# Optimization experiments

Hardware: AMD Instinct MI355X
Metric: run time of the kernel (lower is better)

## Reference

```python
import jax, jax.numpy as jnp
import numpy as np

B, D_IN, U, E = 8192, 1024, 1024, 16

def setup_inputs() -> dict:
    key = jax.random.key(0)
    k1, k2, k3, k4 = jax.random.split(key, 4)
    inputs = jax.random.normal(k1, (B, D_IN), dtype=jnp.float32)
    # type_prob: probability over entity types per example, [B, E, 1]
    tp = jax.random.uniform(k2, (B, E, 1), dtype=jnp.float32)
    type_prob = tp / jnp.sum(tp, axis=1, keepdims=True)
    # Stacked per-entity Dense params: W [E, D_IN, U], b [E, U]
    scale = 1.0 / np.sqrt(D_IN)
    W = jax.random.normal(k3, (E, D_IN, U), dtype=jnp.float32) * scale
    b = jax.random.normal(k4, (E, U), dtype=jnp.float32) * 0.01
    return {"inputs": inputs, "type_prob": type_prob, "W": W, "b": b}

def reference(inputs, type_prob, W, b):
    # Per-entity Dense, batched as one einsum: [B, E, U]
    logits = jnp.einsum('bd,edu->beu', inputs, W) + b
    probs = jax.nn.softmax(logits, axis=-1)  # softmax over wp_units, per entity
    # transpose to [B, U, E], matmul with type_prob [B, E, 1], reduce_sum last axis
    # == weighted combine over entities: [B, U]
    result = jnp.einsum('beu,be->bu', probs, type_prob[..., 0])
    return result
```

## Files before the change

kernel.cpp:

```cpp
#include <hip/hip_runtime.h>
#include <hip/hip_bf16.h>
#include <hip/hip_fp16.h>
#include <stdint.h>

typedef _Float16 f16;
typedef _Float16 f16x4 __attribute__((ext_vector_type(4)));
typedef _Float16 f16x8 __attribute__((ext_vector_type(8)));
typedef float f32x4 __attribute__((ext_vector_type(4)));

#define NB 8192
#define ND 1024
#define NU 1024
#define NE 16

__global__ __launch_bounds__(256) void k_transpose_cast(const float* __restrict__ W,
                                                        f16* __restrict__ WT) {
  __shared__ f16 tile[64][68];
  const int e = blockIdx.z;
  const int u0 = blockIdx.x * 64;
  const int d0 = blockIdx.y * 64;
  const int t = threadIdx.x;
  const int r = t >> 4;
  const int c = (t & 15) << 2;
  const float* src = W + (size_t)e * ND * NU;
  f16* dst = WT + (size_t)e * NU * ND;
#pragma unroll
  for (int i = 0; i < 4; ++i) {
    const int rr = r + i * 16;
    const float4 v = *(const float4*)(src + (size_t)(d0 + rr) * NU + (u0 + c));
    tile[rr][c + 0] = (f16)v.x;
    tile[rr][c + 1] = (f16)v.y;
    tile[rr][c + 2] = (f16)v.z;
    tile[rr][c + 3] = (f16)v.w;
  }
  __syncthreads();
#pragma unroll
  for (int i = 0; i < 4; ++i) {
    const int rr = r + i * 16;
    f16x4 h;
    h[0] = tile[c + 0][rr];
    h[1] = tile[c + 1][rr];
    h[2] = tile[c + 2][rr];
    h[3] = tile[c + 3][rr];
    *(f16x4*)(dst + (size_t)(u0 + rr) * ND + (d0 + c)) = h;
  }
}

__global__ __launch_bounds__(256) void k_cast_x(const float* __restrict__ X,
                                                f16* __restrict__ Xh) {
  const size_t i = ((size_t)blockIdx.x * 256 + threadIdx.x) * 8;
  const float4 v0 = *(const float4*)(X + i);
  const float4 v1 = *(const float4*)(X + i + 4);
  f16x8 h;
  h[0] = (f16)v0.x; h[1] = (f16)v0.y; h[2] = (f16)v0.z; h[3] = (f16)v0.w;
  h[4] = (f16)v1.x; h[5] = (f16)v1.y; h[6] = (f16)v1.z; h[7] = (f16)v1.w;
  *(f16x8*)(Xh + i) = h;
}


typedef __attribute__((address_space(3))) void lds_void_t;
typedef __attribute__((address_space(1))) const void gbl_void_t;

__device__ __forceinline__ void gload16(const void* g, void* l) {
  __builtin_amdgcn_global_load_lds((gbl_void_t*)g, (lds_void_t*)l, 16, 0, 0);
}

#define GSTAGE(buf, kk)                                                        \
  {                                                                            \
    _Pragma("unroll") for (int i_ = 0; i_ < 4; ++i_) {                         \
      const unsigned s_ = i_ * 512 + t;                                        \
      const unsigned row_ = s_ >> 3, ch_ = s_ & 7;                             \
      const unsigned sch_ = ch_ ^ (row_ & 7);                                  \
      const unsigned lb_ = (i_ * 512 + (t & ~63u)) * 16;                       \
      gload16(Ag + (size_t)row_ * 2048 + (size_t)(kk) * 128 + sch_ * 16,       \
              smem + (buf) * 32768 + lb_);                                     \
      gload16(Bg + (size_t)row_ * 2048 + (size_t)(kk) * 128 + sch_ * 16,       \
              smem + 65536 + (buf) * 32768 + lb_);                             \
    }                                                                          \
  }

#define GCOMPUTE(buf)                                                          \
  _Pragma("unroll") for (int ks_ = 0; ks_ < 2; ++ks_) {                        \
    f16x8 bfr_[4];                                                             \
    _Pragma("unroll") for (int nb_ = 0; nb_ < 4; ++nb_) {                      \
      const unsigned U_ = wc * 64 + nb_ * 16 + ln;                             \
      const unsigned ch_ = (unsigned)(ks_ * 4 + g) ^ (U_ & 7);                 \
      bfr_[nb_] =                                                              \
          *(const f16x8*)(smem + 65536 + (buf) * 32768 + U_ * 128 + ch_ * 16); \
    }                                                                          \
    _Pragma("unroll") for (int mb_ = 0; mb_ < 8; ++mb_) {                      \
      const unsigned R_ = wr * 128 + mb_ * 16 + ln;                            \
      const unsigned ch_ = (unsigned)(ks_ * 4 + g) ^ (R_ & 7);                 \
      const f16x8 af_ =                                                        \
          *(const f16x8*)(smem + (buf) * 32768 + R_ * 128 + ch_ * 16);         \
      _Pragma("unroll") for (int nb_ = 0; nb_ < 4; ++nb_) {                    \
        acc[mb_][nb_] = __builtin_amdgcn_mfma_f32_16x16x32_f16(                \
            af_, bfr_[nb_], acc[mb_][nb_], 0, 0, 0);                           \
      }                                                                        \
    }                                                                          \
  }

__global__ __launch_bounds__(512, 2) void k_gemm_exp(const f16* __restrict__ Xc,
                                                     const f16* __restrict__ WT,
                                                     const float* __restrict__ BIAS,
                                                     f16* __restrict__ P,
                                                     float* __restrict__ S4,
                                                     int MTs, int CR) {
  __shared__ alignas(16) unsigned char smem[131072];

  const int t = threadIdx.x;
  const int w = t >> 6;
  const int l = t & 63;
  const int g = l >> 4;
  const int ln = l & 15;
  const int wr = w >> 2;
  const int wc = w & 3;

  const int bid = blockIdx.x;
  const int xcd = bid & 7;
  const int j = bid >> 3;
  const int ntl = j >> MTs;
  const int mt = j & ((1 << MTs) - 1);
  const int nt = xcd * 8 + ntl;

  const char* Ag = (const char*)Xc + (size_t)mt * 256 * 2048;
  const char* Bg = (const char*)WT + (size_t)nt * 256 * 2048;

  f32x4 acc[8][4];
#pragma unroll
  for (int mb = 0; mb < 8; ++mb)
#pragma unroll
    for (int nb = 0; nb < 4; ++nb) acc[mb][nb] = (f32x4){0.f, 0.f, 0.f, 0.f};

  GSTAGE(0, 0);
  __syncthreads();
#pragma unroll 1
  for (int kk = 0; kk < 16; ++kk) {
    const int buf = kk & 1;
    if (kk < 15) GSTAGE(buf ^ 1, kk + 1);
    __builtin_amdgcn_s_setprio(1);
    GCOMPUTE(buf);
    __builtin_amdgcn_s_setprio(0);
    __syncthreads();
  }

  float bv[4];
  const float* bp = BIAS + ((size_t)(nt >> 2) << 10) + (nt & 3) * 256 + wc * 64 + ln;
#pragma unroll
  for (int nb = 0; nb < 4; ++nb) bv[nb] = bp[nb * 16];

  float* red = (float*)smem;
  f16* Prow = P + (size_t)(mt * 256 + wr * 128) * 16384 + (size_t)nt * 256 + wc * 64 + ln;

#pragma unroll
  for (int mb = 0; mb < 8; ++mb) {
    float rs[4] = {0.f, 0.f, 0.f, 0.f};
#pragma unroll
    for (int nb = 0; nb < 4; ++nb) {
#pragma unroll
      for (int r = 0; r < 4; ++r) {
        const float p = __expf(acc[mb][nb][r] + bv[nb]);
        rs[r] += p;
        Prow[(size_t)(mb * 16 + g * 4 + r) * 16384 + nb * 16] = (f16)p;
      }
    }
#pragma unroll
    for (int r = 0; r < 4; ++r) {
      float v = rs[r];
      v += __shfl_xor(v, 1);
      v += __shfl_xor(v, 2);
      v += __shfl_xor(v, 4);
      v += __shfl_xor(v, 8);
      if (ln == 0) red[(wr * 128 + mb * 16 + g * 4 + r) * 4 + wc] = v;
    }
  }
  __syncthreads();
  if (t < 256) {
    const float s = (red[t * 4 + 0] + red[t * 4 + 1]) + (red[t * 4 + 2] + red[t * 4 + 3]);
    S4[(size_t)nt * CR + mt * 256 + t] = s;
  }
}

__global__ __launch_bounds__(512) void k_combine(const f16* __restrict__ P,
                                                 const float* __restrict__ TP,
                                                 const float* __restrict__ S4,
                                                 float* __restrict__ OUT,
                                                 int RB, int CR) {
  __shared__ float c_s[4][16];
  const int t = threadIdx.x;
  const int blk = blockIdx.x;
  if (t < 64) {
    const int rr = t >> 4, e = t & 15;
    const int bl = blk * 4 + rr;
    float S = 0.f;
#pragma unroll
    for (int q = 0; q < 4; ++q) S += S4[(size_t)(e * 4 + q) * CR + bl];
    c_s[rr][e] = TP[(size_t)(RB + bl) * NE + e] / S;
  }
  __syncthreads();
  const int rl = t >> 7;
  const int bl = blk * 4 + rl;
  const int u0 = (t & 127) * 8;
  float a[8] = {0.f, 0.f, 0.f, 0.f, 0.f, 0.f, 0.f, 0.f};
  const f16* Pb = P + (size_t)bl * 16384 + u0;
#pragma unroll
  for (int e = 0; e < NE; ++e) {
    const float c = c_s[rl][e];
    const f16x8 pv = *(const f16x8*)(Pb + e * 1024);
#pragma unroll
    for (int jj = 0; jj < 8; ++jj) a[jj] += c * (float)pv[jj];
  }
  float* op = OUT + (size_t)(RB + bl) * NU + u0;
  *(float4*)(op) = (float4){a[0], a[1], a[2], a[3]};
  *(float4*)(op + 4) = (float4){a[4], a[5], a[6], a[7]};
}

#define BM 64
#define BUH 512
#define NRT 128
#define WT_BYTES ((size_t)NE * NU * ND * 2)
#define SUMS_FLOATS ((size_t)NE * NRT * 2 * 64)
#define FLG_INTS ((size_t)NE * NRT * 2)

#define LOADB(F, soff)                                   \
  {                                                      \
    const char* p_ = wtc + (soff) + vbase;               \
    F[0] = *(const f16x8*)(p_);                          \
    F[1] = *(const f16x8*)(p_ + 1 * 16 * ND * 2);        \
    F[2] = *(const f16x8*)(p_ + 2 * 16 * ND * 2);        \
    F[3] = *(const f16x8*)(p_ + 3 * 16 * ND * 2);        \
  }

#define MFMA_HALF(F, kbyte)                                                         \
  {                                                                                 \
    const f16x8 a0 = *(const f16x8*)(A_s + (ln + 0) * 2064 + g * 16 + (kbyte));     \
    const f16x8 a1 = *(const f16x8*)(A_s + (ln + 16) * 2064 + g * 16 + (kbyte));    \
    const f16x8 a2 = *(const f16x8*)(A_s + (ln + 32) * 2064 + g * 16 + (kbyte));    \
    const f16x8 a3 = *(const f16x8*)(A_s + (ln + 48) * 2064 + g * 16 + (kbyte));    \
    _Pragma("unroll") for (int n_ = 0; n_ < 4; ++n_) {                              \
      acc[0][n_] = __builtin_amdgcn_mfma_f32_16x16x32_f16(a0, F[n_], acc[0][n_], 0, 0, 0); \
      acc[1][n_] = __builtin_amdgcn_mfma_f32_16x16x32_f16(a1, F[n_], acc[1][n_], 0, 0, 0); \
      acc[2][n_] = __builtin_amdgcn_mfma_f32_16x16x32_f16(a2, F[n_], acc[2][n_], 0, 0, 0); \
      acc[3][n_] = __builtin_amdgcn_mfma_f32_16x16x32_f16(a3, F[n_], acc[3][n_], 0, 0, 0); \
    }                                                                               \
  }

__device__ __forceinline__ size_t wt_soff(int L) {
  L = (L > 511) ? 511 : L;
  return (size_t)(L >> 5) * ((size_t)NU * ND * 2) + (size_t)(L & 31) * 64;
}

__global__ __launch_bounds__(512, 2) void k_proj(const float* __restrict__ X,
                                                 const float* __restrict__ TP,
                                                 const f16* __restrict__ WT,
                                                 const float* __restrict__ BIAS,
                                                 float* __restrict__ OUT,
                                                 float* __restrict__ SUMS,
                                                 int* __restrict__ FLG) {
  __shared__ alignas(16) unsigned char lds[132096 + 4096 + 2048 + 256];
  unsigned char* A_s = lds;
  float* tp_s = (float*)(lds + 132096);
  float* reds = (float*)(lds + 132096 + 4096);
  float* sums_s = (float*)(lds + 132096 + 4096 + 2048);

  const int t = threadIdx.x;
  const int w = t >> 6;
  const int l = t & 63;
  const int g = l >> 4;
  const int ln = l & 15;
  const int bid = blockIdx.x;
  const int rt = bid >> 1;
  const int uh = bid & 1;
  const int b0 = rt * BM;
  const int c0 = uh * BUH;

#pragma unroll
  for (int i = 0; i < 32; ++i) {
    const int idx = (i * 512 + t) << 2;
    const int row = idx >> 10;
    const int col = idx & 1023;
    const float4 v = *(const float4*)(X + (size_t)(b0 + row) * ND + col);
    f16x4 h;
    h[0] = (f16)v.x; h[1] = (f16)v.y; h[2] = (f16)v.z; h[3] = (f16)v.w;
    *(f16x4*)(A_s + row * 2064 + (col << 1)) = h;
  }
  tp_s[t] = TP[(size_t)(b0 + (t >> 4)) * NE + (t & 15)];
  tp_s[512 + t] = TP[(size_t)(b0 + 32 + (t >> 4)) * NE + (t & 15)];
  __syncthreads();

  f32x4 out_acc[4][4];
#pragma unroll
  for (int m = 0; m < 4; ++m)
#pragma unroll
    for (int n = 0; n < 4; ++n) out_acc[m][n] = (f32x4){0.f, 0.f, 0.f, 0.f};

  const char* wtc = (const char*)WT;
  const unsigned vbase = ((unsigned)(c0 + w * 64 + ln) * ND + g * 8) * 2;

  f16x8 F0[4], F1[4], F2[4], F3[4];
  LOADB(F0, wt_soff(0));
  LOADB(F1, wt_soff(1));
  LOADB(F2, wt_soff(2));

  for (int e = 0; e < NE; ++e) {
    f32x4 acc[4][4];
#pragma unroll
    for (int m = 0; m < 4; ++m)
#pragma unroll
      for (int n = 0; n < 4; ++n) acc[m][n] = (f32x4){0.f, 0.f, 0.f, 0.f};

    const int Le = e * 32;
#pragma unroll 1
    for (int gi = 0; gi < 7; ++gi) {
      const int L = Le + gi * 4;
      const int kb = gi * 4 * 64;
      LOADB(F3, wt_soff(L + 3));
      MFMA_HALF(F0, kb + 0);
      LOADB(F0, wt_soff(L + 4));
      MFMA_HALF(F1, kb + 64);
      LOADB(F1, wt_soff(L + 5));
      MFMA_HALF(F2, kb + 128);
      LOADB(F2, wt_soff(L + 6));
      MFMA_HALF(F3, kb + 192);
    }
    LOADB(F3, wt_soff(Le + 31));
    MFMA_HALF(F0, 28 * 64);
    LOADB(F0, wt_soff(Le + 32));
    MFMA_HALF(F1, 29 * 64);
    LOADB(F1, wt_soff(Le + 33));
    MFMA_HALF(F2, 30 * 64);
    LOADB(F2, wt_soff(Le + 34));
    MFMA_HALF(F3, 31 * 64);

    const float* bp = BIAS + (size_t)e * NU + c0 + w * 64 + ln;
    float bv[4];
#pragma unroll
    for (int n = 0; n < 4; ++n) bv[n] = bp[n * 16];

    float rs[4][4];
#pragma unroll
    for (int m = 0; m < 4; ++m)
#pragma unroll
      for (int r = 0; r < 4; ++r) rs[m][r] = 0.f;
#pragma unroll
    for (int m = 0; m < 4; ++m)
#pragma unroll
      for (int n = 0; n < 4; ++n)
#pragma unroll
        for (int r = 0; r < 4; ++r) {
          const float p = __expf(acc[m][n][r] + bv[n]);
          acc[m][n][r] = p;
          rs[m][r] += p;
        }
#pragma unroll
    for (int m = 0; m < 4; ++m)
#pragma unroll
      for (int r = 0; r < 4; ++r) {
        float v = rs[m][r];
        v += __shfl_xor(v, 1, 64);
        v += __shfl_xor(v, 2, 64);
        v += __shfl_xor(v, 4, 64);
        v += __shfl_xor(v, 8, 64);
        rs[m][r] = v;
      }
    if (ln == 0) {
#pragma unroll
      for (int m = 0; m < 4; ++m)
#pragma unroll
        for (int r = 0; r < 4; ++r) reds[(m * 16 + g * 4 + r) * 8 + w] = rs[m][r];
    }
    __syncthreads();

    const int pairbase = (e * NRT + rt) * 2;
    float myS = 0.f;
    if (t < 64) {
      const float* rp = reds + t * 8;
      myS = ((rp[0] + rp[1]) + (rp[2] + rp[3])) + ((rp[4] + rp[5]) + (rp[6] + rp[7]));
      __hip_atomic_store(&SUMS[(size_t)(pairbase + uh) * 64 + t], myS,
                         __ATOMIC_RELAXED, __HIP_MEMORY_SCOPE_AGENT);
    }
    __syncthreads();
    if (t == 0) {
      __threadfence();
      __hip_atomic_store(&FLG[pairbase + uh], 1, __ATOMIC_RELEASE, __HIP_MEMORY_SCOPE_AGENT);
      int spin = 0;
      while (__hip_atomic_load(&FLG[pairbase + (uh ^ 1)], __ATOMIC_ACQUIRE,
                               __HIP_MEMORY_SCOPE_AGENT) == 0 &&
             spin < 400000) {
        __builtin_amdgcn_s_sleep(2);
        ++spin;
      }
    }
    __syncthreads();
    if (t < 64) {
      const float ps = __hip_atomic_load(&SUMS[(size_t)(pairbase + (uh ^ 1)) * 64 + t],
                                         __ATOMIC_RELAXED, __HIP_MEMORY_SCOPE_AGENT);
      sums_s[t] = myS + ps;
    }
    __syncthreads();

#pragma unroll
    for (int m = 0; m < 4; ++m)
#pragma unroll
      for (int r = 0; r < 4; ++r) {
        const int row = m * 16 + g * 4 + r;
        const float scale = tp_s[row * 16 + e] * __builtin_amdgcn_rcpf(sums_s[row]);
#pragma unroll
        for (int n = 0; n < 4; ++n) out_acc[m][n][r] += scale * acc[m][n][r];
      }
  }

#pragma unroll
  for (int m = 0; m < 4; ++m)
#pragma unroll
    for (int r = 0; r < 4; ++r) {
      float* op = OUT + (size_t)(b0 + m * 16 + g * 4 + r) * NU + c0 + w * 64 + ln;
#pragma unroll
      for (int n = 0; n < 4; ++n) op[n * 16] = out_acc[m][n][r];
    }
}

extern "C" void kernel_launch(void* const* d_in, const int* in_sizes, int n_in,
                              void* d_out, int out_size, void* d_ws, size_t ws_size,
                              hipStream_t stream) {
  const float* X = (const float*)d_in[0];
  const float* TP = (const float*)d_in[1];
  const float* W = (const float*)d_in[2];
  const float* BIAS = (const float*)d_in[3];
  float* OUT = (float*)d_out;

  const size_t XH_BYTES = (size_t)NB * ND * 2;
  const size_t FIXED = WT_BYTES + XH_BYTES;

  int CR = 0;
  for (int cr = NB; cr >= 256; cr >>= 1) {
    const size_t need = FIXED + (size_t)cr * 16384 * 2 + (size_t)cr * 64 * 4;
    if (ws_size >= need) { CR = cr; break; }
  }

  if (CR > 0) {
    f16* WT = (f16*)d_ws;
    f16* Xh = (f16*)((char*)d_ws + WT_BYTES);
    float* S4 = (float*)((char*)d_ws + FIXED);
    f16* P = (f16*)((char*)d_ws + FIXED + (size_t)CR * 64 * 4);

    k_transpose_cast<<<dim3(16, 16, 16), dim3(256), 0, stream>>>(W, WT);
    k_cast_x<<<dim3(4096), dim3(256), 0, stream>>>(X, Xh);

    const int MT = CR / 256;
    int MTs = 0;
    while ((1 << MTs) < MT) ++MTs;
    const int nch = NB / CR;
    for (int ch = 0; ch < nch; ++ch) {
      const int RB = ch * CR;
      k_gemm_exp<<<dim3(MT * 64), dim3(512), 0, stream>>>(
          Xh + (size_t)RB * ND, WT, BIAS, P, S4, MTs, CR);
      k_combine<<<dim3(CR / 4), dim3(512), 0, stream>>>(P, TP, S4, OUT, RB, CR);
    }
  } else {
    f16* WT = (f16*)d_ws;
    float* SUMS = (float*)((char*)d_ws + WT_BYTES);
    int* FLG = (int*)((char*)d_ws + WT_BYTES + SUMS_FLOATS * 4);

    hipMemsetAsync(FLG, 0, FLG_INTS * sizeof(int), stream);
    k_transpose_cast<<<dim3(16, 16, 16), dim3(256), 0, stream>>>(W, WT);
    k_proj<<<dim3(256), dim3(512), 0, stream>>>(X, TP, WT, BIAS, OUT, SUMS, FLG);
  }
}
```

Measured before the change: 382.1 us.

## Split GEMM K-loop into half-tile staged quadrants with fine-grained waitcnt pipelining

Replaces the simple double-buffered GEMM main loop with a schedule that stages A and B in half-tiles and interleaves global-to-LDS loads for tiles k+1 and k+2 between four MFMA quadrant blocks. Register fragments for A and B are loaded explicitly, and manual vmcnt/lgkmcnt waits plus barriers replace __syncthreads. The goal is to hide global-load and LDS latency behind MFMA work, in the style of the HipKittens 8-wave ping-pong. It adds many barriers and hand-managed wait counts, which can be fragile and may increase sync overhead.

```diff
diff --git a/kernel.cpp b/kernel.cpp
--- a/kernel.cpp
+++ b/kernel.cpp
@@ -65,40 +65,49 @@
   __builtin_amdgcn_global_load_lds((gbl_void_t*)g, (lds_void_t*)l, 16, 0, 0);
 }
 
-#define GSTAGE(buf, kk)                                                        \
-  {                                                                            \
-    _Pragma("unroll") for (int i_ = 0; i_ < 4; ++i_) {                         \
-      const unsigned s_ = i_ * 512 + t;                                        \
-      const unsigned row_ = s_ >> 3, ch_ = s_ & 7;                             \
-      const unsigned sch_ = ch_ ^ (row_ & 7);                                  \
-      const unsigned lb_ = (i_ * 512 + (t & ~63u)) * 16;                       \
-      gload16(Ag + (size_t)row_ * 2048 + (size_t)(kk) * 128 + sch_ * 16,       \
-              smem + (buf) * 32768 + lb_);                                     \
-      gload16(Bg + (size_t)row_ * 2048 + (size_t)(kk) * 128 + sch_ * 16,       \
-              smem + 65536 + (buf) * 32768 + lb_);                             \
-    }                                                                          \
-  }
-
-#define GCOMPUTE(buf)                                                          \
-  _Pragma("unroll") for (int ks_ = 0; ks_ < 2; ++ks_) {                        \
-    f16x8 bfr_[4];                                                             \
-    _Pragma("unroll") for (int nb_ = 0; nb_ < 4; ++nb_) {                      \
-      const unsigned U_ = wc * 64 + nb_ * 16 + ln;                             \
-      const unsigned ch_ = (unsigned)(ks_ * 4 + g) ^ (U_ & 7);                 \
-      bfr_[nb_] =                                                              \
-          *(const f16x8*)(smem + 65536 + (buf) * 32768 + U_ * 128 + ch_ * 16); \
-    }                                                                          \
-    _Pragma("unroll") for (int mb_ = 0; mb_ < 8; ++mb_) {                      \
-      const unsigned R_ = wr * 128 + mb_ * 16 + ln;                            \
-      const unsigned ch_ = (unsigned)(ks_ * 4 + g) ^ (R_ & 7);                 \
-      const f16x8 af_ =                                                        \
-          *(const f16x8*)(smem + (buf) * 32768 + R_ * 128 + ch_ * 16);         \
-      _Pragma("unroll") for (int nb_ = 0; nb_ < 4; ++nb_) {                    \
-        acc[mb_][nb_] = __builtin_amdgcn_mfma_f32_16x16x32_f16(                \
-            af_, bfr_[nb_], acc[mb_][nb_], 0, 0, 0);                           \
-      }                                                                        \
-    }                                                                          \
-  }
+#define WAIT_VM6() do { asm volatile("s_waitcnt vmcnt(6)" ::: "memory"); \
+                        __builtin_amdgcn_sched_barrier(0); } while (0)
+#define WAIT_VM0() do { asm volatile("s_waitcnt vmcnt(0)" ::: "memory"); \
+                        __builtin_amdgcn_sched_barrier(0); } while (0)
+#define WAIT_LGKM0() do { asm volatile("s_waitcnt lgkmcnt(0)" ::: "memory"); \
+                          __builtin_amdgcn_sched_barrier(0); } while (0)
+#define BARR() do { asm volatile("" ::: "memory"); __builtin_amdgcn_s_barrier(); \
+                    asm volatile("" ::: "memory"); } while (0)
+
+#define STAGEH(op, h, kt, buf)                                                  \
+  {                                                                             \
+    const char* src_ = (op) ? Bg : Ag;                                          \
+    _Pragma("unroll") for (int i_ = 0; i_ < 2; ++i_) {                          \
+      const unsigned s_ = i_ * 512 + t;                                         \
+      const unsigned row_ = (h) * 128 + (s_ >> 3);                              \
+      const unsigned sch_ = (s_ & 7) ^ (row_ & 7);                              \
+      const unsigned lb_ = (unsigned)(buf) * 65536 + (op) * 32768 +             \
+                           (h) * 16384 + (i_ * 512 + (t & ~63u)) * 16;          \
+      gload16(src_ + (size_t)row_ * 2048 + (size_t)(kt) * 128 + sch_ * 16,      \
+              smem + lb_);                                                      \
+    }                                                                           \
+  }
+
+#define LDA(mb0, buf)                                                           \
+  _Pragma("unroll") for (int j_ = 0; j_ < 4; ++j_)                              \
+    _Pragma("unroll") for (int ks_ = 0; ks_ < 2; ++ks_)                         \
+      a[j_][ks_] = *(const f16x8*)(smem + (unsigned)(buf) * 65536 +             \
+                     wr * 16384 + (((mb0) + j_) * 16 + ln) * 128 +              \
+                     (((unsigned)(ks_ * 4 + g)) ^ (ln & 7u)) * 16);
+
+#define LDB(buf)                                                                \
+  _Pragma("unroll") for (int n_ = 0; n_ < 4; ++n_)                              \
+    _Pragma("unroll") for (int ks_ = 0; ks_ < 2; ++ks_)                         \
+      b[n_][ks_] = *(const f16x8*)(smem + (unsigned)(buf) * 65536 + 32768 +     \
+                     (wc >> 1) * 16384 + ((wc & 1) * 64 + n_ * 16 + ln) * 128 + \
+                     (((unsigned)(ks_ * 4 + g)) ^ (ln & 7u)) * 16);
+
+#define QUAD(mb0, n0)                                                           \
+  _Pragma("unroll") for (int j_ = 0; j_ < 4; ++j_)                              \
+    _Pragma("unroll") for (int n_ = 0; n_ < 2; ++n_)                            \
+      _Pragma("unroll") for (int ks_ = 0; ks_ < 2; ++ks_)                       \
+        acc[(mb0) + j_][(n0) + n_] = __builtin_amdgcn_mfma_f32_16x16x32_f16(    \
+            a[j_][ks_], b[(n0) + n_][ks_], acc[(mb0) + j_][(n0) + n_], 0, 0, 0);
 
 __global__ __launch_bounds__(512, 2) void k_gemm_exp(const f16* __restrict__ Xc,
                                                      const f16* __restrict__ WT,
@@ -132,17 +141,59 @@
 #pragma unroll
     for (int nb = 0; nb < 4; ++nb) acc[mb][nb] = (f32x4){0.f, 0.f, 0.f, 0.f};
 
-  GSTAGE(0, 0);
+  f16x8 a[4][2], b[4][2];
+
+  STAGEH(0, 0, 0, 0); STAGEH(0, 1, 0, 0); STAGEH(1, 0, 0, 0); STAGEH(1, 1, 0, 0);
+  STAGEH(1, 0, 1, 1); STAGEH(1, 1, 1, 1); STAGEH(0, 0, 1, 1);
+  WAIT_VM6();
+  BARR();
+
+#pragma unroll 1
+  for (int k = 0; k < 15; ++k) {
+    const int cur = k & 1, nxt = cur ^ 1;
+    LDA(0, cur);
+    LDB(cur);
+    STAGEH(0, 1, k + 1, nxt);
+    BARR();
+    WAIT_LGKM0();
+    __builtin_amdgcn_s_setprio(1);
+    QUAD(0, 0);
+    __builtin_amdgcn_s_setprio(0);
+    BARR();
+    if (k < 14) STAGEH(1, 0, k + 2, cur);
+    BARR();
+    __builtin_amdgcn_s_setprio(1);
+    QUAD(0, 2);
+    __builtin_amdgcn_s_setprio(0);
+    BARR();
+    LDA(4, cur);
+    if (k < 14) STAGEH(1, 1, k + 2, cur);
+    BARR();
+    WAIT_LGKM0();
+    __builtin_amdgcn_s_setprio(1);
+    QUAD(4, 2);
+    __builtin_amdgcn_s_setprio(0);
+    BARR();
+    if (k < 14) STAGEH(0, 0, k + 2, cur);
+    BARR();
+    __builtin_amdgcn_s_setprio(1);
+    QUAD(4, 0);
+    __builtin_amdgcn_s_setprio(0);
+    WAIT_VM6();
+    BARR();
+  }
+  WAIT_VM0();
+  BARR();
+  LDA(0, 1);
+  LDB(1);
+  WAIT_LGKM0();
+  QUAD(0, 0);
+  QUAD(0, 2);
+  LDA(4, 1);
+  WAIT_LGKM0();
+  QUAD(4, 2);
+  QUAD(4, 0);
   __syncthreads();
-#pragma unroll 1
-  for (int kk = 0; kk < 16; ++kk) {
-    const int buf = kk & 1;
-    if (kk < 15) GSTAGE(buf ^ 1, kk + 1);
-    __builtin_amdgcn_s_setprio(1);
-    GCOMPUTE(buf);
-    __builtin_amdgcn_s_setprio(0);
-    __syncthreads();
-  }
 
   float bv[4];
   const float* bp = BIAS + ((size_t)(nt >> 2) << 10) + (nt & 3) * 256 + wc * 64 + ln;
@@ -201,18 +252,18 @@
   const int rl = t >> 7;
   const int bl = blk * 4 + rl;
   const int u0 = (t & 127) * 8;
-  float a[8] = {0.f, 0.f, 0.f, 0.f, 0.f, 0.f, 0.f, 0.f};
+  float acm[8] = {0.f, 0.f, 0.f, 0.f, 0.f, 0.f, 0.f, 0.f};
   const f16* Pb = P + (size_t)bl * 16384 + u0;
 #pragma unroll
   for (int e = 0; e < NE; ++e) {
     const float c = c_s[rl][e];
     const f16x8 pv = *(const f16x8*)(Pb + e * 1024);
 #pragma unroll
-    for (int jj = 0; jj < 8; ++jj) a[jj] += c * (float)pv[jj];
+    for (int jj = 0; jj < 8; ++jj) acm[jj] += c * (float)pv[jj];
   }
   float* op = OUT + (size_t)(RB + bl) * NU + u0;
-  *(float4*)(op) = (float4){a[0], a[1], a[2], a[3]};
-  *(float4*)(op + 4) = (float4){a[4], a[5], a[6], a[7]};
+  *(float4*)(op) = (float4){acm[0], acm[1], acm[2], acm[3]};
+  *(float4*)(op + 4) = (float4){acm[4], acm[5], acm[6], acm[7]};
 }
 
 #define BM 64
```

Measured after the change: 382.3 us. No clear change (+0.0%).
